# Optimization experiments

Measured on AMD Instinct MI355X. Metric: run time of the kernel, lower is better.

The kernel has to match this reference:

```python
import jax, jax.numpy as jnp
import numpy as np

N = 60000      # n_total_medical_code (graph nodes)
E = 600000     # nnz of sparse adjacency
D = 128        # args.dynamic_size
FEAT = 128     # args.feature_size
B = 256        # len(codeid)
P = 10000      # n_patient
ALPHA = 0.1
EPS = 1e-12    # F.normalize eps


def _l2norm(x):
    # F.normalize(x) : L2 over dim=1
    n = jnp.sqrt(jnp.sum(x * x, axis=1, keepdims=True))
    return x / jnp.maximum(n, EPS)


def _gcn_layer(x, W, edge_row, edge_col, edge_val, init_x):
    # support = X @ W ; out = A @ support (sparse) ; alpha-blend residual ; ReLU
    support = x @ W                                    # [N, D]
    msgs = support[edge_col] * edge_val[:, None]       # [E, D] gather + scale
    agg = jax.ops.segment_sum(msgs, edge_row, num_segments=N)  # [N, D] scatter-add
    out = ALPHA * agg + (1.0 - ALPHA) * init_x
    return jax.nn.relu(out)


def setup_inputs() -> dict:
    key = jax.random.key(0)
    ks = jax.random.split(key, 16)
    stdv = 1.0 / np.sqrt(D)
    in_rnn = D + 1 + FEAT  # 257
    stdv_rnn = 1.0 / np.sqrt(D)
    return {
        "code_dynamic": jax.random.normal(ks[0], (N, D), jnp.float32),
        "init_code_dynamic": jax.random.normal(ks[1], (N, D), jnp.float32),
        "patient_dynamic": jax.random.normal(ks[2], (P, D), jnp.float32),
        "timediffs": jax.random.normal(ks[3], (B, 1), jnp.float32),
        "features": jax.random.normal(ks[4], (B, FEAT), jnp.float32),
        "edge_val": jax.random.uniform(ks[5], (E,), jnp.float32),
        "W1": jax.random.uniform(ks[6], (D, D), jnp.float32, -stdv, stdv),
        "W2": jax.random.uniform(ks[7], (D, D), jnp.float32, -stdv, stdv),
        "W_ih": jax.random.uniform(ks[8], (D, in_rnn), jnp.float32, -stdv_rnn, stdv_rnn),
        "b_ih": jax.random.uniform(ks[9], (D,), jnp.float32, -stdv_rnn, stdv_rnn),
        "W_hh": jax.random.uniform(ks[10], (D, D), jnp.float32, -stdv_rnn, stdv_rnn),
        "b_hh": jax.random.uniform(ks[11], (D,), jnp.float32, -stdv_rnn, stdv_rnn),
        "edge_row": jax.random.randint(ks[12], (E,), 0, N, jnp.int32),
        "edge_col": jax.random.randint(ks[13], (E,), 0, N, jnp.int32),
        "codeid": jax.random.randint(ks[14], (B,), 0, N, jnp.int32),
        "patientid": 0,
    }


def reference(code_dynamic, init_code_dynamic, patient_dynamic, timediffs, features,
              edge_val, W1, W2, W_ih, b_ih, W_hh, b_hh,
              edge_row, edge_col, codeid, patientid):
    # select == 'code_update' branch. x = code_dynamic.clone().detach()
    x = jax.lax.stop_gradient(code_dynamic)
    x = _gcn_layer(x, W1, edge_row, edge_col, edge_val, init_code_dynamic)
    # dropout: inference mode -> identity
    x = _gcn_layer(x, W2, edge_row, edge_col, edge_val, init_code_dynamic)
    code_embed = x[codeid]                               # [B, D]
    patient_embed = jnp.broadcast_to(patient_dynamic[patientid][None, :], (B, D))
    input1 = jnp.concatenate([patient_embed, timediffs, features], axis=1)  # [B, D+1+FEAT]
    # RNNCell (tanh): h' = tanh(x W_ih^T + b_ih + h W_hh^T + b_hh)
    h = jnp.tanh(input1 @ W_ih.T + b_ih + code_embed @ W_hh.T + b_hh)
    return _l2norm(h)
```

## Files before the change

### kernel.cpp

```cpp
#include <hip/hip_runtime.h>
#include <math.h>

#define GD 128
#define ELLW 64
#define NSEG 512
#define NT 8

__global__ __launch_bounds__(256) void passA(const int* __restrict__ codeid, int B,
                                             const int* __restrict__ erow,
                                             const int* __restrict__ ecol, int E,
                                             int N, int MAXH,
                                             int* __restrict__ list1,
                                             int* __restrict__ bcnt,
                                             int* __restrict__ cntarr,
                                             const float* __restrict__ patient,
                                             const float* __restrict__ W_ih,
                                             const float* __restrict__ b_ih,
                                             const float* __restrict__ b_hh,
                                             const int* __restrict__ patientid,
                                             float* __restrict__ pc) {
    extern __shared__ unsigned int bm[];
    __shared__ int lcnt;
    int t = threadIdx.x;
    int words = (N + 31) >> 5;
    for (int i = t; i < words; i += 256) bm[i] = 0;
    if (t == 0) lcnt = 0;
    __syncthreads();
    for (int i = t; i < B; i += 256) {
        int c = codeid[i];
        atomicOr(&bm[c >> 5], 1u << (c & 31));
    }
    __syncthreads();

    if (blockIdx.x == gridDim.x - 1 && t < GD) {
        int pid = patientid[0];
        const float* wih = W_ih + (size_t)t * 257;
        const float* pp = patient + (size_t)pid * GD;
        float a0 = 0.f, a1 = 0.f;
#pragma unroll 8
        for (int k = 0; k < GD; k += 2) {
            a0 += pp[k] * wih[k];
            a1 += pp[k + 1] * wih[k + 1];
        }
        pc[t] = b_ih[t] + b_hh[t] + a0 + a1;
    }

    int gid = blockIdx.x * 256 + t, gs = gridDim.x * 256;
    for (int i = gid; i < N; i += gs) cntarr[i] = 0;
    int* seg = list1 + (size_t)blockIdx.x * MAXH;
    for (int e = gid; e < E; e += gs) {
        int r = erow[e];
        if ((bm[r >> 5] >> (r & 31)) & 1u) {
            int idx = atomicAdd(&lcnt, 1);
            seg[idx] = ecol[e];
        }
    }
    __syncthreads();
    if (t == 0) bcnt[blockIdx.x] = lcnt;
}

__global__ __launch_bounds__(256) void passB(const int* __restrict__ erow,
                                             const int* __restrict__ ecol,
                                             const float* __restrict__ ev, int E,
                                             const int* __restrict__ codeid, int B,
                                             const int* __restrict__ list1,
                                             const int* __restrict__ bcnt,
                                             int MAXH, int N,
                                             int* __restrict__ cnt,
                                             int* __restrict__ ellc,
                                             float* __restrict__ ellv) {
    extern __shared__ unsigned int bm[];
    int t = threadIdx.x;
    int words = (N + 31) >> 5;
    for (int i = t; i < words; i += 256) bm[i] = 0;
    __syncthreads();
    for (int i = t; i < B; i += 256) {
        int c = codeid[i];
        atomicOr(&bm[c >> 5], 1u << (c & 31));
    }
    for (int s = t; s < NSEG; s += 256) {
        int c = bcnt[s];
        const int* seg = list1 + (size_t)s * MAXH;
        for (int k = 0; k < c; ++k) {
            int u = seg[k];
            atomicOr(&bm[u >> 5], 1u << (u & 31));
        }
    }
    __syncthreads();

    int gid = blockIdx.x * 256 + t, gs = gridDim.x * 256;
    for (int e = gid; e < E; e += gs) {
        int r = erow[e];
        if ((bm[r >> 5] >> (r & 31)) & 1u) {
            int idx = atomicAdd(&cnt[r], 1);
            if (idx < ELLW) {
                ellc[(size_t)r * ELLW + idx] = ecol[e];
                ellv[(size_t)r * ELLW + idx] = ev[e];
            }
        }
    }
}

__global__ __launch_bounds__(512) void fused12(const float* __restrict__ X,
                                               const float* __restrict__ W1,
                                               const float* __restrict__ W2,
                                               const float* __restrict__ init,
                                               const int* __restrict__ cnt,
                                               const int* __restrict__ ellc,
                                               const float* __restrict__ ellv,
                                               const int* __restrict__ codeid,
                                               const float* __restrict__ timediffs,
                                               const float* __restrict__ features,
                                               const float* __restrict__ W_ih,
                                               const float* __restrict__ W_hh,
                                               const float* __restrict__ pc,
                                               float* __restrict__ out) {
    __shared__ int   sec[ELLW];
    __shared__ float sev[ELLW];
    __shared__ int   ncnt[NT];
    __shared__ int   nec[NT][ELLW];
    __shared__ float nev[NT][ELLW];
    __shared__ float gxall[NT][GD];
    __shared__ float p2[4][GD];
    __shared__ float gx2[GD];
    __shared__ float feat[GD];
    __shared__ float ce[GD];
    __shared__ float red[GD];

    int b = blockIdx.x, t = threadIdx.x;
    int sub = t >> 7, j = t & 127;
    int cid = codeid[b];
    int c = cnt[cid]; if (c > ELLW) c = ELLW;

    if (t < c) { sec[t] = ellc[(size_t)cid * ELLW + t]; sev[t] = ellv[(size_t)cid * ELLW + t]; }
    if (t < GD) feat[t] = features[(size_t)b * GD + t];
    __syncthreads();

    float a2 = 0.f;
    for (int tb = 0; tb < c; tb += NT) {
        int nt = c - tb; if (nt > NT) nt = NT;
        if (t < NT) ncnt[t] = (t < nt) ? min(cnt[sec[tb + t]], ELLW) : 0;
        __syncthreads();
        {
            int i = t >> 6, k = t & 63;
            bool ok = (k < ncnt[i]);
            nec[i][k] = ok ? ellc[(size_t)sec[tb + i] * ELLW + k] : 0;
            nev[i][k] = ok ? ellv[(size_t)sec[tb + i] * ELLW + k] : 0.f;
        }
        __syncthreads();

        int ia = sub, ib = sub + 4;
        int cm = max(ncnt[ia], ncnt[ib]);
        cm = (cm + 3) & ~3;
        float ga0 = 0.f, ga1 = 0.f, ga2 = 0.f, ga3 = 0.f;
        float gb0 = 0.f, gb1 = 0.f, gb2 = 0.f, gb3 = 0.f;
        for (int k = 0; k < cm; k += 4) {
            ga0 += nev[ia][k]     * X[(size_t)nec[ia][k]     * GD + j];
            ga1 += nev[ia][k + 1] * X[(size_t)nec[ia][k + 1] * GD + j];
            ga2 += nev[ia][k + 2] * X[(size_t)nec[ia][k + 2] * GD + j];
            ga3 += nev[ia][k + 3] * X[(size_t)nec[ia][k + 3] * GD + j];
            gb0 += nev[ib][k]     * X[(size_t)nec[ib][k]     * GD + j];
            gb1 += nev[ib][k + 1] * X[(size_t)nec[ib][k + 1] * GD + j];
            gb2 += nev[ib][k + 2] * X[(size_t)nec[ib][k + 2] * GD + j];
            gb3 += nev[ib][k + 3] * X[(size_t)nec[ib][k + 3] * GD + j];
        }
        gxall[ia][j] = (ga0 + ga1) + (ga2 + ga3);
        gxall[ib][j] = (gb0 + gb1) + (gb2 + gb3);
        __syncthreads();

        float xa0 = 0.f, xa1 = 0.f, xb0 = 0.f, xb1 = 0.f;
#pragma unroll 4
        for (int k = 0; k < GD; k += 2) {
            float w0 = W1[(size_t)k * GD + j];
            float w1 = W1[(size_t)(k + 1) * GD + j];
            xa0 += gxall[ia][k] * w0; xa1 += gxall[ia][k + 1] * w1;
            xb0 += gxall[ib][k] * w0; xb1 += gxall[ib][k + 1] * w1;
        }
        if (tb + ia < c) {
            float x1v = fmaxf(0.1f * (xa0 + xa1)
                              + 0.9f * init[(size_t)sec[tb + ia] * GD + j], 0.f);
            a2 += sev[tb + ia] * x1v;
        }
        if (tb + ib < c) {
            float x1v = fmaxf(0.1f * (xb0 + xb1)
                              + 0.9f * init[(size_t)sec[tb + ib] * GD + j], 0.f);
            a2 += sev[tb + ib] * x1v;
        }
    }
    p2[sub][j] = a2;
    __syncthreads();
    if (t < GD) gx2[t] = (p2[0][t] + p2[1][t]) + (p2[2][t] + p2[3][t]);
    __syncthreads();

    {
        int kb = sub << 5;
        float a0 = 0.f, a1 = 0.f, b2 = 0.f, b3 = 0.f;
#pragma unroll 8
        for (int k = 0; k < 32; k += 4) {
            a0 += gx2[kb + k]     * W2[(size_t)(kb + k)     * GD + j];
            a1 += gx2[kb + k + 1] * W2[(size_t)(kb + k + 1) * GD + j];
            b2 += gx2[kb + k + 2] * W2[(size_t)(kb + k + 2) * GD + j];
            b3 += gx2[kb + k + 3] * W2[(size_t)(kb + k + 3) * GD + j];
        }
        p2[sub][j] = (a0 + a1) + (b2 + b3);
    }
    __syncthreads();
    if (t < GD)
        ce[t] = fmaxf(0.1f * ((p2[0][t] + p2[1][t]) + (p2[2][t] + p2[3][t]))
                      + 0.9f * init[(size_t)cid * GD + t], 0.f);
    __syncthreads();

    {
        const float* wih = W_ih + (size_t)j * 257;
        const float* whh = W_hh + (size_t)j * GD;
        int kb = sub << 5;
        float a0 = (sub == 0) ? (pc[j] + timediffs[b] * wih[GD]) : 0.f;
        float a1 = 0.f, b2 = 0.f, b3 = 0.f;
#pragma unroll 8
        for (int k = 0; k < 32; k += 4) {
            a0 += feat[kb + k]     * wih[129 + kb + k];
            a1 += feat[kb + k + 1] * wih[129 + kb + k + 1];
            b2 += feat[kb + k + 2] * wih[129 + kb + k + 2];
            b3 += feat[kb + k + 3] * wih[129 + kb + k + 3];
        }
#pragma unroll 8
        for (int k = 0; k < 32; k += 4) {
            a0 += ce[kb + k]     * whh[kb + k];
            a1 += ce[kb + k + 1] * whh[kb + k + 1];
            b2 += ce[kb + k + 2] * whh[kb + k + 2];
            b3 += ce[kb + k + 3] * whh[kb + k + 3];
        }
        p2[sub][j] = (a0 + a1) + (b2 + b3);
    }
    __syncthreads();
    float h = 0.f;
    if (t < GD) {
        h = tanhf((p2[0][t] + p2[1][t]) + (p2[2][t] + p2[3][t]));
        red[t] = h * h;
    }
    __syncthreads();
    for (int s = 64; s > 0; s >>= 1) {
        if (t < s) red[t] += red[t + s];
        __syncthreads();
    }
    if (t < GD) {
        float nrm = fmaxf(sqrtf(red[0]), 1e-12f);
        out[(size_t)b * GD + t] = h / nrm;
    }
}


extern "C" void kernel_launch(void* const* d_in, const int* in_sizes, int n_in,
                              void* d_out, int out_size, void* d_ws, size_t ws_size,
                              hipStream_t stream) {
    const float* code_dynamic = (const float*)d_in[0];
    const float* init_cd      = (const float*)d_in[1];
    const float* patient      = (const float*)d_in[2];
    const float* timediffs    = (const float*)d_in[3];
    const float* features     = (const float*)d_in[4];
    const float* edge_val     = (const float*)d_in[5];
    const float* W1           = (const float*)d_in[6];
    const float* W2           = (const float*)d_in[7];
    const float* W_ih         = (const float*)d_in[8];
    const float* b_ih         = (const float*)d_in[9];
    const float* W_hh         = (const float*)d_in[10];
    const float* b_hh         = (const float*)d_in[11];
    const int* edge_row       = (const int*)d_in[12];
    const int* edge_col       = (const int*)d_in[13];
    const int* codeid         = (const int*)d_in[14];
    const int* patientid      = (const int*)d_in[15];

    int N = in_sizes[0] / GD;
    int E = in_sizes[5];
    int B = in_sizes[14];

    int MAXH = 256 * ((E + NSEG * 256 - 1) / (NSEG * 256));

    int*   ellc   = (int*)d_ws;
    float* ellv   = (float*)(ellc + (size_t)N * ELLW);
    int*   cntarr = (int*)(ellv + (size_t)N * ELLW);
    int*   list1  = cntarr + N;
    int*   bcnt   = list1 + (size_t)NSEG * MAXH;
    float* pcbuf  = (float*)(bcnt + NSEG);

    size_t bmBytes = (size_t)((N + 31) / 32) * sizeof(unsigned int);

    passA<<<NSEG, 256, bmBytes, stream>>>(codeid, B, edge_row, edge_col, E,
                                          N, MAXH, list1, bcnt, cntarr,
                                          patient, W_ih, b_ih, b_hh, patientid, pcbuf);
    passB<<<NSEG, 256, bmBytes, stream>>>(edge_row, edge_col, edge_val, E,
                                          codeid, B, list1, bcnt, MAXH, N,
                                          cntarr, ellc, ellv);
    fused12<<<B, 512, 0, stream>>>(code_dynamic, W1, W2, init_cd,
                                   cntarr, ellc, ellv, codeid, timediffs, features,
                                   W_ih, W_hh, pcbuf, (float*)d_out);
}
```

Measured before the change: 44.41 us.

## Vectorize edge-row scans with int4 loads and process 16 neighbors per tile

The edge filtering passes now read edge_row as int4 and test four edges per thread iteration, and the count array is zeroed with int4 stores. The per-code fused kernel raises the neighbor tile from 8 to 16, so each thread accumulates four neighbor rows at once with 2-way unrolling instead of two rows with 4-way unrolling. This halves the synchronisation rounds per code and shares the W1 loads across more rows. In exchange it uses more registers and shared memory, and it assumes N is a multiple of 4 for the vectorized zeroing, with no tail loop for the remainder.

```diff
diff --git a/kernel.cpp b/kernel.cpp
--- a/kernel.cpp
+++ b/kernel.cpp
@@ -4,7 +4,7 @@
 #define GD 128
 #define ELLW 64
 #define NSEG 512
-#define NT 8
+#define NT 16
 
 __global__ __launch_bounds__(256) void passA(const int* __restrict__ codeid, int B,
                                              const int* __restrict__ erow,
@@ -46,14 +46,25 @@
     }
 
     int gid = blockIdx.x * 256 + t, gs = gridDim.x * 256;
-    for (int i = gid; i < N; i += gs) cntarr[i] = 0;
+    {
+        int4* z = (int4*)cntarr;
+        int n4 = N >> 2;
+        for (int i = gid; i < n4; i += gs) z[i] = make_int4(0, 0, 0, 0);
+    }
     int* seg = list1 + (size_t)blockIdx.x * MAXH;
-    for (int e = gid; e < E; e += gs) {
+    const int4* erow4 = (const int4*)erow;
+    int E4 = E >> 2;
+    for (int q = gid; q < E4; q += gs) {
+        int4 r4 = erow4[q];
+        int e = q << 2;
+        if ((bm[r4.x >> 5] >> (r4.x & 31)) & 1u) seg[atomicAdd(&lcnt, 1)] = ecol[e];
+        if ((bm[r4.y >> 5] >> (r4.y & 31)) & 1u) seg[atomicAdd(&lcnt, 1)] = ecol[e + 1];
+        if ((bm[r4.z >> 5] >> (r4.z & 31)) & 1u) seg[atomicAdd(&lcnt, 1)] = ecol[e + 2];
+        if ((bm[r4.w >> 5] >> (r4.w & 31)) & 1u) seg[atomicAdd(&lcnt, 1)] = ecol[e + 3];
+    }
+    for (int e = (E4 << 2) + gid; e < E; e += gs) {
         int r = erow[e];
-        if ((bm[r >> 5] >> (r & 31)) & 1u) {
-            int idx = atomicAdd(&lcnt, 1);
-            seg[idx] = ecol[e];
-        }
+        if ((bm[r >> 5] >> (r & 31)) & 1u) seg[atomicAdd(&lcnt, 1)] = ecol[e];
     }
     __syncthreads();
     if (t == 0) bcnt[blockIdx.x] = lcnt;
@@ -89,7 +100,25 @@
     __syncthreads();
 
     int gid = blockIdx.x * 256 + t, gs = gridDim.x * 256;
-    for (int e = gid; e < E; e += gs) {
+    const int4* erow4 = (const int4*)erow;
+    int E4 = E >> 2;
+    for (int q = gid; q < E4; q += gs) {
+        int4 r4 = erow4[q];
+        int e = q << 2;
+        int rr[4] = { r4.x, r4.y, r4.z, r4.w };
+#pragma unroll 4
+        for (int u = 0; u < 4; ++u) {
+            int r = rr[u];
+            if ((bm[r >> 5] >> (r & 31)) & 1u) {
+                int idx = atomicAdd(&cnt[r], 1);
+                if (idx < ELLW) {
+                    ellc[(size_t)r * ELLW + idx] = ecol[e + u];
+                    ellv[(size_t)r * ELLW + idx] = ev[e + u];
+                }
+            }
+        }
+    }
+    for (int e = (E4 << 2) + gid; e < E; e += gs) {
         int r = erow[e];
         if ((bm[r >> 5] >> (r & 31)) & 1u) {
             int idx = atomicAdd(&cnt[r], 1);
@@ -142,39 +171,46 @@
         if (t < NT) ncnt[t] = (t < nt) ? min(cnt[sec[tb + t]], ELLW) : 0;
         __syncthreads();
         {
-            int i = t >> 6, k = t & 63;
-            bool ok = (k < ncnt[i]);
-            nec[i][k] = ok ? ellc[(size_t)sec[tb + i] * ELLW + k] : 0;
-            nev[i][k] = ok ? ellv[(size_t)sec[tb + i] * ELLW + k] : 0.f;
+            for (int idx = t; idx < NT * ELLW; idx += 512) {
+                int i = idx >> 6, k = idx & 63;
+                bool ok = (k < ncnt[i]);
+                nec[i][k] = ok ? ellc[(size_t)sec[tb + i] * ELLW + k] : 0;
+                nev[i][k] = ok ? ellv[(size_t)sec[tb + i] * ELLW + k] : 0.f;
+            }
         }
         __syncthreads();
 
-        int ia = sub, ib = sub + 4;
-        int cm = max(ncnt[ia], ncnt[ib]);
-        cm = (cm + 3) & ~3;
-        float ga0 = 0.f, ga1 = 0.f, ga2 = 0.f, ga3 = 0.f;
-        float gb0 = 0.f, gb1 = 0.f, gb2 = 0.f, gb3 = 0.f;
-        for (int k = 0; k < cm; k += 4) {
+        int ia = sub, ib = sub + 4, ic = sub + 8, id = sub + 12;
+        int cm = max(max(ncnt[ia], ncnt[ib]), max(ncnt[ic], ncnt[id]));
+        cm = (cm + 1) & ~1;
+        float ga0 = 0.f, ga1 = 0.f, gb0 = 0.f, gb1 = 0.f;
+        float gc0 = 0.f, gc1 = 0.f, gd0 = 0.f, gd1 = 0.f;
+        for (int k = 0; k < cm; k += 2) {
             ga0 += nev[ia][k]     * X[(size_t)nec[ia][k]     * GD + j];
             ga1 += nev[ia][k + 1] * X[(size_t)nec[ia][k + 1] * GD + j];
-            ga2 += nev[ia][k + 2] * X[(size_t)nec[ia][k + 2] * GD + j];
-            ga3 += nev[ia][k + 3] * X[(size_t)nec[ia][k + 3] * GD + j];
             gb0 += nev[ib][k]     * X[(size_t)nec[ib][k]     * GD + j];
             gb1 += nev[ib][k + 1] * X[(size_t)nec[ib][k + 1] * GD + j];
-            gb2 += nev[ib][k + 2] * X[(size_t)nec[ib][k + 2] * GD + j];
-            gb3 += nev[ib][k + 3] * X[(size_t)nec[ib][k + 3] * GD + j];
-        }
-        gxall[ia][j] = (ga0 + ga1) + (ga2 + ga3);
-        gxall[ib][j] = (gb0 + gb1) + (gb2 + gb3);
+            gc0 += nev[ic][k]     * X[(size_t)nec[ic][k]     * GD + j];
+            gc1 += nev[ic][k + 1] * X[(size_t)nec[ic][k + 1] * GD + j];
+            gd0 += nev[id][k]     * X[(size_t)nec[id][k]     * GD + j];
+            gd1 += nev[id][k + 1] * X[(size_t)nec[id][k + 1] * GD + j];
+        }
+        gxall[ia][j] = ga0 + ga1;
+        gxall[ib][j] = gb0 + gb1;
+        gxall[ic][j] = gc0 + gc1;
+        gxall[id][j] = gd0 + gd1;
         __syncthreads();
 
         float xa0 = 0.f, xa1 = 0.f, xb0 = 0.f, xb1 = 0.f;
+        float xc0 = 0.f, xc1 = 0.f, xd0 = 0.f, xd1 = 0.f;
 #pragma unroll 4
         for (int k = 0; k < GD; k += 2) {
             float w0 = W1[(size_t)k * GD + j];
             float w1 = W1[(size_t)(k + 1) * GD + j];
             xa0 += gxall[ia][k] * w0; xa1 += gxall[ia][k + 1] * w1;
             xb0 += gxall[ib][k] * w0; xb1 += gxall[ib][k + 1] * w1;
+            xc0 += gxall[ic][k] * w0; xc1 += gxall[ic][k + 1] * w1;
+            xd0 += gxall[id][k] * w0; xd1 += gxall[id][k + 1] * w1;
         }
         if (tb + ia < c) {
             float x1v = fmaxf(0.1f * (xa0 + xa1)
@@ -185,6 +221,16 @@
             float x1v = fmaxf(0.1f * (xb0 + xb1)
                               + 0.9f * init[(size_t)sec[tb + ib] * GD + j], 0.f);
             a2 += sev[tb + ib] * x1v;
+        }
+        if (tb + ic < c) {
+            float x1v = fmaxf(0.1f * (xc0 + xc1)
+                              + 0.9f * init[(size_t)sec[tb + ic] * GD + j], 0.f);
+            a2 += sev[tb + ic] * x1v;
+        }
+        if (tb + id < c) {
+            float x1v = fmaxf(0.1f * (xd0 + xd1)
+                              + 0.9f * init[(size_t)sec[tb + id] * GD + j], 0.f);
+            a2 += sev[tb + id] * x1v;
         }
     }
     p2[sub][j] = a2;
@@ -274,7 +320,10 @@
     int E = in_sizes[5];
     int B = in_sizes[14];
 
-    int MAXH = 256 * ((E + NSEG * 256 - 1) / (NSEG * 256));
+    int gs = NSEG * 256;
+    int E4 = E >> 2;
+    int chunksPerThread = (E4 + gs - 1) / gs;
+    int MAXH = 1024 * chunksPerThread + 16;
 
     int*   ellc   = (int*)d_ws;
     float* ellv   = (float*)(ellc + (size_t)N * ELLW);
```

After: 43.68 us. No clear change (-1.7%).
